# Kernel tuning notes

Measured on AMD Instinct MI355X. Metric: run time of the kernel, lower is better.

The kernel has to match this reference:

```python
import jax, jax.numpy as jnp
import numpy as np

NUM_EXPERTS = 64
TOP_K = 2


def setup_inputs() -> dict:
    key = jax.random.key(0)
    k1, k2 = jax.random.split(key)
    hidden_states = jax.random.normal(k1, (4, 4096, 4096), dtype=jnp.float32)
    W = jax.random.normal(k2, (NUM_EXPERTS, 4096), dtype=jnp.float32) * 0.02
    return {"hidden_states": hidden_states, "W": W}


def reference(hidden_states, W):
    # Eval-mode MoE routing: gate GEMM -> softmax -> top-k -> renorm -> sort/bincount dispatch.
    B, S, H = hidden_states.shape
    x = hidden_states.reshape(-1, H)                       # (T, H), T = B*S
    router_logits = jnp.einsum('th,eh->te', x, W)          # (T, E)
    routing_probs = jax.nn.softmax(router_logits, axis=-1)
    routing_weights, selected_experts = jax.lax.top_k(routing_probs, TOP_K)  # (T, K)
    routing_weights = routing_weights / routing_weights.sum(axis=-1, keepdims=True)
    # grouped-GEMM dispatch indices
    flat_experts = selected_experts.reshape(-1)            # (T*K,)
    gather_indices = jnp.argsort(flat_experts, stable=True)  # stable counting-sort permutation
    m_sizes = jnp.bincount(flat_experts, length=NUM_EXPERTS)
    return (routing_weights.reshape(-1), selected_experts, m_sizes, gather_indices)
```

## Files before the change

### kernel.cpp

```cpp
#include <hip/hip_runtime.h>
#include <hip/hip_bf16.h>
#include <math.h>

#define T_TOKENS 16384
#define H_DIM    4096
#define N_EXP    64
#define KSPLIT   4
#define KCHUNK   (H_DIM / KSPLIT)
#define MTILE    128
#define BK       32
#define NB       128

__global__ __launch_bounds__(256, 2)
void gate_gemm(const float* __restrict__ x, const float* __restrict__ W,
               float* __restrict__ part) {
  __shared__ float xs[MTILE][BK + 1];
  __shared__ float wsm[N_EXP][BK + 1];
  const int bx = blockIdx.x;
  const int kc = bx >> 7;
  const int tb = (bx & 127) * MTILE;
  const int t  = threadIdx.x;
  const int tokgrp = t & 15;
  const int expgrp = t >> 4;
  const int lrow = t >> 3;
  const int lcol = (t & 7) * 4;
  const int k0 = kc * KCHUNK;

  float acc[8][4];
  #pragma unroll
  for (int i = 0; i < 8; ++i)
    #pragma unroll
    for (int j = 0; j < 4; ++j) acc[i][j] = 0.f;

  for (int kb = 0; kb < KCHUNK; kb += BK) {
    __syncthreads();
    #pragma unroll
    for (int r = 0; r < 4; ++r) {
      const int row = lrow + 32 * r;
      const float4 v = *reinterpret_cast<const float4*>(
          &x[(size_t)(tb + row) * H_DIM + k0 + kb + lcol]);
      xs[row][lcol + 0] = v.x; xs[row][lcol + 1] = v.y;
      xs[row][lcol + 2] = v.z; xs[row][lcol + 3] = v.w;
    }
    #pragma unroll
    for (int r = 0; r < 2; ++r) {
      const int row = lrow + 32 * r;
      const float4 v = *reinterpret_cast<const float4*>(
          &W[(size_t)row * H_DIM + k0 + kb + lcol]);
      wsm[row][lcol + 0] = v.x; wsm[row][lcol + 1] = v.y;
      wsm[row][lcol + 2] = v.z; wsm[row][lcol + 3] = v.w;
    }
    __syncthreads();
    #pragma unroll 8
    for (int kk = 0; kk < BK; ++kk) {
      float xa[8], wa[4];
      #pragma unroll
      for (int i = 0; i < 8; ++i) xa[i] = xs[tokgrp * 8 + i][kk];
      #pragma unroll
      for (int j = 0; j < 4; ++j) wa[j] = wsm[expgrp * 4 + j][kk];
      #pragma unroll
      for (int i = 0; i < 8; ++i)
        #pragma unroll
        for (int j = 0; j < 4; ++j)
          acc[i][j] = fmaf(xa[i], wa[j], acc[i][j]);
    }
  }
  float* dst = part + (size_t)kc * T_TOKENS * N_EXP;
  #pragma unroll
  for (int i = 0; i < 8; ++i) {
    const int tok = tb + tokgrp * 8 + i;
    float4 v = make_float4(acc[i][0], acc[i][1], acc[i][2], acc[i][3]);
    *reinterpret_cast<float4*>(&dst[(size_t)tok * N_EXP + expgrp * 4]) = v;
  }
}

__global__ __launch_bounds__(256)
void softmax_top2(const float* __restrict__ part, float* __restrict__ out,
                  int* __restrict__ sel) {
  const int lane = threadIdx.x & 63;
  const int tok  = blockIdx.x * 4 + (threadIdx.x >> 6);
  const size_t base = (size_t)tok * N_EXP + lane;
  float l = 0.f;
  #pragma unroll
  for (int c = 0; c < KSPLIT; ++c)
    l += part[(size_t)c * T_TOKENS * N_EXP + base];
  float m = l;
  #pragma unroll
  for (int o = 32; o >= 1; o >>= 1) m = fmaxf(m, __shfl_xor(m, o));
  const float e = expf(l - m);
  float s = e;
  #pragma unroll
  for (int o = 32; o >= 1; o >>= 1) s += __shfl_xor(s, o);
  const float p = e / s;
  float v1 = p; int i1 = lane;
  #pragma unroll
  for (int o = 32; o >= 1; o >>= 1) {
    const float ov = __shfl_xor(v1, o); const int oi = __shfl_xor(i1, o);
    if (ov > v1 || (ov == v1 && oi < i1)) { v1 = ov; i1 = oi; }
  }
  float v2 = (lane == i1) ? -INFINITY : p; int i2 = lane;
  #pragma unroll
  for (int o = 32; o >= 1; o >>= 1) {
    const float ov = __shfl_xor(v2, o); const int oi = __shfl_xor(i2, o);
    if (ov > v2 || (ov == v2 && oi < i2)) { v2 = ov; i2 = oi; }
  }
  if (lane == 0) {
    const float den = v1 + v2;
    out[2 * tok]     = v1 / den;
    out[2 * tok + 1] = v2 / den;
    out[2 * T_TOKENS + 2 * tok]     = (float)i1;
    out[2 * T_TOKENS + 2 * tok + 1] = (float)i2;
    sel[2 * tok]     = i1;
    sel[2 * tok + 1] = i2;
  }
}

__global__ __launch_bounds__(256)
void hist_kernel(const int* __restrict__ sel, int* __restrict__ hist) {
  __shared__ int h[N_EXP];
  const int t = threadIdx.x;
  if (t < N_EXP) h[t] = 0;
  __syncthreads();
  atomicAdd(&h[sel[blockIdx.x * 256 + t]], 1);
  __syncthreads();
  if (t < N_EXP) hist[blockIdx.x * N_EXP + t] = h[t];
}

__global__ __launch_bounds__(64)
void scan_kernel(const int* __restrict__ hist, int* __restrict__ boff,
                 float* __restrict__ out_msizes) {
  const int e = threadIdx.x;
  int total = 0;
  for (int b = 0; b < NB; ++b) total += hist[b * N_EXP + e];
  out_msizes[e] = (float)total;
  int incl = total;
  #pragma unroll
  for (int o = 1; o < 64; o <<= 1) {
    const int v = __shfl_up(incl, o);
    if (e >= o) incl += v;
  }
  int run = incl - total;
  for (int b = 0; b < NB; ++b) {
    boff[b * N_EXP + e] = run;
    run += hist[b * N_EXP + e];
  }
}

__global__ __launch_bounds__(256)
void scatter_kernel(const int* __restrict__ sel, const int* __restrict__ boff,
                    float* __restrict__ out_gather) {
  __shared__ int le[256];
  __shared__ int off[N_EXP];
  const int t = threadIdx.x;
  const int i = blockIdx.x * 256 + t;
  const int e = sel[i];
  le[t] = e;
  if (t < N_EXP) off[t] = boff[blockIdx.x * N_EXP + t];
  __syncthreads();
  int rank = 0;
  for (int j = 0; j < 256; ++j)
    rank += (j < t) & (le[j] == e);
  out_gather[off[e] + rank] = (float)i;
}

extern "C" void kernel_launch(void* const* d_in, const int* in_sizes, int n_in,
                              void* d_out, int out_size, void* d_ws, size_t ws_size,
                              hipStream_t stream) {
  const float* x = (const float*)d_in[0];
  const float* W = (const float*)d_in[1];
  float* out = (float*)d_out;

  float* part = (float*)d_ws;
  int*   sel  = (int*)(part + (size_t)KSPLIT * T_TOKENS * N_EXP);
  int*   hist = sel + 2 * T_TOKENS;
  int*   boff = hist + NB * N_EXP;

  hipLaunchKernelGGL(gate_gemm, dim3((T_TOKENS / MTILE) * KSPLIT), dim3(256), 0, stream,
                     x, W, part);
  hipLaunchKernelGGL(softmax_top2, dim3(T_TOKENS / 4), dim3(256), 0, stream,
                     part, out, sel);
  hipLaunchKernelGGL(hist_kernel, dim3(NB), dim3(256), 0, stream, sel, hist);
  hipLaunchKernelGGL(scan_kernel, dim3(1), dim3(64), 0, stream,
                     boff ? hist : hist, boff, out + 4 * T_TOKENS);
  hipLaunchKernelGGL(scatter_kernel, dim3(NB), dim3(256), 0, stream,
                     sel, boff, out + 4 * T_TOKENS + N_EXP);
}
```

Baseline: 525.9 us.

## Fuse gate GEMM, softmax/top-2 and histogram into one kernel with per-lane tokens

Replaces the split-K tiled GEMM, the separate softmax/top-2 kernel and the histogram kernel with one fused kernel. Each lane owns one token and keeps 64 expert accumulators in registers, and the 16 waves of a block split the hidden dimension. W is read straight from global memory at the same address across a wave (broadcast), and x is prefetched with double-buffered float4 loads. Partial sums are reduced through shared memory, then softmax/top-2 runs in-block and the histogram is built with global atomics after a memset. This removes the split-K partial-sum buffer round trip and two launches, and the scan kernel now stages the histogram in LDS. The cost is high register pressure from 64 accumulators at 1024 threads per block, uncoalesced per-token x row reads, and an added reduction step.

```diff
diff --git a/kernel.cpp b/kernel.cpp
--- a/kernel.cpp
+++ b/kernel.cpp
@@ -5,144 +5,153 @@
 #define T_TOKENS 16384
 #define H_DIM    4096
 #define N_EXP    64
-#define KSPLIT   4
-#define KCHUNK   (H_DIM / KSPLIT)
-#define MTILE    128
-#define BK       32
+#define WAVES    16
+#define KRANGE   (H_DIM / WAVES)
+#define KB       16
 #define NB       128
 
-__global__ __launch_bounds__(256, 2)
-void gate_gemm(const float* __restrict__ x, const float* __restrict__ W,
-               float* __restrict__ part) {
-  __shared__ float xs[MTILE][BK + 1];
-  __shared__ float wsm[N_EXP][BK + 1];
-  const int bx = blockIdx.x;
-  const int kc = bx >> 7;
-  const int tb = (bx & 127) * MTILE;
-  const int t  = threadIdx.x;
-  const int tokgrp = t & 15;
-  const int expgrp = t >> 4;
-  const int lrow = t >> 3;
-  const int lcol = (t & 7) * 4;
-  const int k0 = kc * KCHUNK;
+__global__ __launch_bounds__(1024, 4)
+void gate_fused(const float* __restrict__ x, const float* __restrict__ W,
+                float* __restrict__ out, int* __restrict__ sel,
+                int* __restrict__ hist) {
+  const int t    = threadIdx.x;
+  const int w    = t >> 6;
+  const int lane = t & 63;
+  const int tokbase = blockIdx.x * 64;
+  const int tok  = tokbase + lane;
+  const int k0   = w * KRANGE;
 
-  float acc[8][4];
+  float acc[N_EXP];
   #pragma unroll
-  for (int i = 0; i < 8; ++i)
+  for (int e = 0; e < N_EXP; ++e) acc[e] = 0.f;
+
+  const float* xrow = x + (size_t)tok * H_DIM + k0;
+  float4 c0 = *(const float4*)(xrow + 0);
+  float4 c1 = *(const float4*)(xrow + 4);
+  float4 c2 = *(const float4*)(xrow + 8);
+  float4 c3 = *(const float4*)(xrow + 12);
+
+  for (int kb = 0; kb < KRANGE; kb += KB) {
+    float4 n0 = c0, n1 = c1, n2 = c2, n3 = c3;
+    const int nxt = kb + KB;
+    if (nxt < KRANGE) {
+      n0 = *(const float4*)(xrow + nxt + 0);
+      n1 = *(const float4*)(xrow + nxt + 4);
+      n2 = *(const float4*)(xrow + nxt + 8);
+      n3 = *(const float4*)(xrow + nxt + 12);
+    }
+    float xv[KB];
+    xv[0]=c0.x; xv[1]=c0.y; xv[2]=c0.z; xv[3]=c0.w;
+    xv[4]=c1.x; xv[5]=c1.y; xv[6]=c1.z; xv[7]=c1.w;
+    xv[8]=c2.x; xv[9]=c2.y; xv[10]=c2.z; xv[11]=c2.w;
+    xv[12]=c3.x; xv[13]=c3.y; xv[14]=c3.z; xv[15]=c3.w;
+
     #pragma unroll
-    for (int j = 0; j < 4; ++j) acc[i][j] = 0.f;
+    for (int e = 0; e < N_EXP; ++e) {
+      const float* wrow = W + (size_t)e * H_DIM + k0 + kb;
+      const float4 w0 = *(const float4*)(wrow + 0);
+      const float4 w1 = *(const float4*)(wrow + 4);
+      const float4 w2 = *(const float4*)(wrow + 8);
+      const float4 w3 = *(const float4*)(wrow + 12);
+      float wv[KB];
+      wv[0]=w0.x; wv[1]=w0.y; wv[2]=w0.z; wv[3]=w0.w;
+      wv[4]=w1.x; wv[5]=w1.y; wv[6]=w1.z; wv[7]=w1.w;
+      wv[8]=w2.x; wv[9]=w2.y; wv[10]=w2.z; wv[11]=w2.w;
+      wv[12]=w3.x; wv[13]=w3.y; wv[14]=w3.z; wv[15]=w3.w;
+      #pragma unroll
+      for (int j = 0; j < KB; ++j)
+        acc[e] = fmaf(xv[j], wv[j], acc[e]);
+    }
+    c0 = n0; c1 = n1; c2 = n2; c3 = n3;
+  }
 
-  for (int kb = 0; kb < KCHUNK; kb += BK) {
+  __shared__ float red[WAVES][64][9];
+  __shared__ float logit[64][65];
+  for (int ec = 0; ec < 8; ++ec) {
     __syncthreads();
     #pragma unroll
-    for (int r = 0; r < 4; ++r) {
-      const int row = lrow + 32 * r;
-      const float4 v = *reinterpret_cast<const float4*>(
-          &x[(size_t)(tb + row) * H_DIM + k0 + kb + lcol]);
-      xs[row][lcol + 0] = v.x; xs[row][lcol + 1] = v.y;
-      xs[row][lcol + 2] = v.z; xs[row][lcol + 3] = v.w;
-    }
-    #pragma unroll
-    for (int r = 0; r < 2; ++r) {
-      const int row = lrow + 32 * r;
-      const float4 v = *reinterpret_cast<const float4*>(
-          &W[(size_t)row * H_DIM + k0 + kb + lcol]);
-      wsm[row][lcol + 0] = v.x; wsm[row][lcol + 1] = v.y;
-      wsm[row][lcol + 2] = v.z; wsm[row][lcol + 3] = v.w;
-    }
+    for (int j = 0; j < 8; ++j) red[w][lane][j] = acc[ec * 8 + j];
     __syncthreads();
-    #pragma unroll 8
-    for (int kk = 0; kk < BK; ++kk) {
-      float xa[8], wa[4];
+    if (t < 512) {
+      const int lr = t >> 3, j = t & 7;
+      float s = 0.f;
       #pragma unroll
-      for (int i = 0; i < 8; ++i) xa[i] = xs[tokgrp * 8 + i][kk];
-      #pragma unroll
-      for (int j = 0; j < 4; ++j) wa[j] = wsm[expgrp * 4 + j][kk];
-      #pragma unroll
-      for (int i = 0; i < 8; ++i)
-        #pragma unroll
-        for (int j = 0; j < 4; ++j)
-          acc[i][j] = fmaf(xa[i], wa[j], acc[i][j]);
+      for (int ww = 0; ww < WAVES; ++ww) s += red[ww][lr][j];
+      logit[lr][ec * 8 + j] = s;
     }
   }
-  float* dst = part + (size_t)kc * T_TOKENS * N_EXP;
-  #pragma unroll
-  for (int i = 0; i < 8; ++i) {
-    const int tok = tb + tokgrp * 8 + i;
-    float4 v = make_float4(acc[i][0], acc[i][1], acc[i][2], acc[i][3]);
-    *reinterpret_cast<float4*>(&dst[(size_t)tok * N_EXP + expgrp * 4]) = v;
+  __syncthreads();
+
+  for (int tt = 0; tt < 4; ++tt) {
+    const int trow = w * 4 + tt;
+    const float l = logit[trow][lane];
+    float m = l;
+    #pragma unroll
+    for (int o = 32; o >= 1; o >>= 1) m = fmaxf(m, __shfl_xor(m, o));
+    const float ex = expf(l - m);
+    float s = ex;
+    #pragma unroll
+    for (int o = 32; o >= 1; o >>= 1) s += __shfl_xor(s, o);
+    const float p = ex / s;
+    float v1 = p; int i1 = lane;
+    #pragma unroll
+    for (int o = 32; o >= 1; o >>= 1) {
+      const float ov = __shfl_xor(v1, o); const int oi = __shfl_xor(i1, o);
+      if (ov > v1 || (ov == v1 && oi < i1)) { v1 = ov; i1 = oi; }
+    }
+    float v2 = (lane == i1) ? -INFINITY : p; int i2 = lane;
+    #pragma unroll
+    for (int o = 32; o >= 1; o >>= 1) {
+      const float ov = __shfl_xor(v2, o); const int oi = __shfl_xor(i2, o);
+      if (ov > v2 || (ov == v2 && oi < i2)) { v2 = ov; i2 = oi; }
+    }
+    if (lane == 0) {
+      const int gtok = tokbase + trow;
+      const float den = v1 + v2;
+      out[2 * gtok]     = v1 / den;
+      out[2 * gtok + 1] = v2 / den;
+      out[2 * T_TOKENS + 2 * gtok]     = (float)i1;
+      out[2 * T_TOKENS + 2 * gtok + 1] = (float)i2;
+      sel[2 * gtok]     = i1;
+      sel[2 * gtok + 1] = i2;
+      atomicAdd(&hist[(gtok >> 7) * N_EXP + i1], 1);
+      atomicAdd(&hist[(gtok >> 7) * N_EXP + i2], 1);
+    }
   }
 }
 
 __global__ __launch_bounds__(256)
-void softmax_top2(const float* __restrict__ part, float* __restrict__ out,
-                  int* __restrict__ sel) {
-  const int lane = threadIdx.x & 63;
-  const int tok  = blockIdx.x * 4 + (threadIdx.x >> 6);
-  const size_t base = (size_t)tok * N_EXP + lane;
-  float l = 0.f;
-  #pragma unroll
-  for (int c = 0; c < KSPLIT; ++c)
-    l += part[(size_t)c * T_TOKENS * N_EXP + base];
-  float m = l;
-  #pragma unroll
-  for (int o = 32; o >= 1; o >>= 1) m = fmaxf(m, __shfl_xor(m, o));
-  const float e = expf(l - m);
-  float s = e;
-  #pragma unroll
-  for (int o = 32; o >= 1; o >>= 1) s += __shfl_xor(s, o);
-  const float p = e / s;
-  float v1 = p; int i1 = lane;
-  #pragma unroll
-  for (int o = 32; o >= 1; o >>= 1) {
-    const float ov = __shfl_xor(v1, o); const int oi = __shfl_xor(i1, o);
-    if (ov > v1 || (ov == v1 && oi < i1)) { v1 = ov; i1 = oi; }
-  }
-  float v2 = (lane == i1) ? -INFINITY : p; int i2 = lane;
-  #pragma unroll
-  for (int o = 32; o >= 1; o >>= 1) {
-    const float ov = __shfl_xor(v2, o); const int oi = __shfl_xor(i2, o);
-    if (ov > v2 || (ov == v2 && oi < i2)) { v2 = ov; i2 = oi; }
-  }
-  if (lane == 0) {
-    const float den = v1 + v2;
-    out[2 * tok]     = v1 / den;
-    out[2 * tok + 1] = v2 / den;
-    out[2 * T_TOKENS + 2 * tok]     = (float)i1;
-    out[2 * T_TOKENS + 2 * tok + 1] = (float)i2;
-    sel[2 * tok]     = i1;
-    sel[2 * tok + 1] = i2;
-  }
-}
-
-__global__ __launch_bounds__(256)
-void hist_kernel(const int* __restrict__ sel, int* __restrict__ hist) {
-  __shared__ int h[N_EXP];
-  const int t = threadIdx.x;
-  if (t < N_EXP) h[t] = 0;
-  __syncthreads();
-  atomicAdd(&h[sel[blockIdx.x * 256 + t]], 1);
-  __syncthreads();
-  if (t < N_EXP) hist[blockIdx.x * N_EXP + t] = h[t];
-}
-
-__global__ __launch_bounds__(64)
 void scan_kernel(const int* __restrict__ hist, int* __restrict__ boff,
                  float* __restrict__ out_msizes) {
-  const int e = threadIdx.x;
-  int total = 0;
-  for (int b = 0; b < NB; ++b) total += hist[b * N_EXP + e];
-  out_msizes[e] = (float)total;
-  int incl = total;
-  #pragma unroll
-  for (int o = 1; o < 64; o <<= 1) {
-    const int v = __shfl_up(incl, o);
-    if (e >= o) incl += v;
+  __shared__ int hs[NB * N_EXP];
+  __shared__ int pt[4][N_EXP];
+  __shared__ int base_s[N_EXP];
+  const int t = threadIdx.x;
+  for (int i = t; i < NB * N_EXP; i += 256) hs[i] = hist[i];
+  __syncthreads();
+  const int e = t & 63, g = t >> 6;
+  int part = 0;
+  for (int c = g * 32; c < g * 32 + 32; ++c) part += hs[c * N_EXP + e];
+  pt[g][e] = part;
+  __syncthreads();
+  if (t < 64) {
+    const int total = pt[0][e] + pt[1][e] + pt[2][e] + pt[3][e];
+    out_msizes[e] = (float)total;
+    int incl = total;
+    #pragma unroll
+    for (int o = 1; o < 64; o <<= 1) {
+      const int v = __shfl_up(incl, o);
+      if (e >= o) incl += v;
+    }
+    base_s[e] = incl - total;
   }
-  int run = incl - total;
-  for (int b = 0; b < NB; ++b) {
-    boff[b * N_EXP + e] = run;
-    run += hist[b * N_EXP + e];
+  __syncthreads();
+  if (t < 64) {
+    int run = base_s[e];
+    for (int c = 0; c < NB; ++c) {
+      boff[c * N_EXP + e] = run;
+      run += hs[c * N_EXP + e];
+    }
   }
 }
 
@@ -170,18 +179,15 @@
   const float* W = (const float*)d_in[1];
   float* out = (float*)d_out;
 
-  float* part = (float*)d_ws;
-  int*   sel  = (int*)(part + (size_t)KSPLIT * T_TOKENS * N_EXP);
-  int*   hist = sel + 2 * T_TOKENS;
-  int*   boff = hist + NB * N_EXP;
+  int* sel  = (int*)d_ws;
+  int* hist = sel + 2 * T_TOKENS;
+  int* boff = hist + NB * N_EXP;
 
-  hipLaunchKernelGGL(gate_gemm, dim3((T_TOKENS / MTILE) * KSPLIT), dim3(256), 0, stream,
-                     x, W, part);
-  hipLaunchKernelGGL(softmax_top2, dim3(T_TOKENS / 4), dim3(256), 0, stream,
-                     part, out, sel);
-  hipLaunchKernelGGL(hist_kernel, dim3(NB), dim3(256), 0, stream, sel, hist);
-  hipLaunchKernelGGL(scan_kernel, dim3(1), dim3(64), 0, stream,
-                     boff ? hist : hist, boff, out + 4 * T_TOKENS);
+  hipMemsetAsync(hist, 0, NB * N_EXP * sizeof(int), stream);
+  hipLaunchKernelGGL(gate_fused, dim3(T_TOKENS / 64), dim3(1024), 0, stream,
+                     x, W, out, sel, hist);
+  hipLaunchKernelGGL(scan_kernel, dim3(1), dim3(256), 0, stream,
+                     hist, boff, out + 4 * T_TOKENS);
   hipLaunchKernelGGL(scatter_kernel, dim3(NB), dim3(256), 0, stream,
                      sel, boff, out + 4 * T_TOKENS + N_EXP);
 }
```

After: 887.1 us. 68.7% more time.
